# Kernel optimization log

Hardware: AMD Instinct MI355X
Metric: run time of the kernel (lower is better)

The kernel has to match this reference:

```python
import jax, jax.numpy as jnp
import numpy as np
from jax import lax

N_EXPERTS = 256
N_GROUP = 8
TOPK_GROUP = 4
TOP_K = 8
AUX_ALPHA = 0.001


def setup_inputs() -> dict:
    key = jax.random.key(0)
    k1, k2 = jax.random.split(key)
    hidden_states = jax.random.normal(k1, (16384, 2048), dtype=jnp.float32)
    weight = jax.random.normal(k2, (N_EXPERTS, 2048), dtype=jnp.float32) * 0.02
    return {"hidden_states": hidden_states, "weight": weight}


def reference(hidden_states, weight):
    n_tokens = hidden_states.shape[0]
    group_size = N_EXPERTS // N_GROUP  # 32

    # gating logits: [N, E]
    logits = jnp.einsum('nh,eh->ne', hidden_states, weight)

    # group-restricted top-k: [N, G, group_size] -> top TOPK_GROUP per group
    group_logits = logits.reshape(n_tokens, N_GROUP, group_size)
    gw, gi = lax.top_k(group_logits, TOPK_GROUP)          # [N, G, tg]
    gw = gw.reshape(n_tokens, N_GROUP * TOPK_GROUP)
    gi = gi.reshape(n_tokens, N_GROUP * TOPK_GROUP)

    # global top-k over the pooled group winners
    topk_weights, ti = lax.top_k(gw, TOP_K)               # [N, K]
    selected_group = ti // TOPK_GROUP
    expert_in_group = jnp.take_along_axis(gi, ti, axis=1)
    topk_idx = selected_group * group_size + expert_in_group  # [N, K]

    # norm_topk_prob=True
    topk_weights = topk_weights / (jnp.sum(topk_weights, axis=-1, keepdims=True) + 1e-20)

    # auxiliary load-balancing loss (training path)
    expert_mask = jax.nn.one_hot(topk_idx.reshape(-1), N_EXPERTS, dtype=jnp.float32)
    expert_counts = expert_mask.mean(axis=0)              # [E]
    expert_probs = jax.nn.softmax(logits, axis=-1).mean(axis=0)  # [E]
    aux_loss = jnp.sum(expert_counts * expert_probs) * AUX_ALPHA

    return topk_idx, topk_weights, aux_loss
```

## Files before the change

kernel.cpp:

```cpp
#include <hip/hip_runtime.h>
#include <math.h>

#define NTOK 16384
#define KD   2048
#define NE   256
#define NCHUNK 128
#define CHUNK_DW 4096
#define TM 16
#define SL 257

__global__ __launch_bounds__(256) void transform_kernel(
    const float* __restrict__ wgt, float* __restrict__ Bt)
{
    const int c    = blockIdx.x >> 2;
    const int qt   = blockIdx.x & 3;
    const int slot = qt * 256 + threadIdx.x;
    const int s    = slot >> 6;
    const int lane = slot & 63;
    const int em   = lane >> 2;
    const int l    = lane & 3;
    const int e    = (s >> 1) * 32 + (s & 1) * 16 + em;
    const float* src = wgt + (size_t)e * KD + 16 * c + l;
    float4 v = make_float4(src[0], src[4], src[8], src[12]);
    *(float4*)(Bt + (size_t)c * CHUNK_DW + slot * 4) = v;
}

typedef __attribute__((address_space(1))) const void GV;
typedef __attribute__((address_space(3))) void LV;
__device__ __forceinline__ void gld_lds16(const float* g, float* l) {
    __builtin_amdgcn_global_load_lds((GV*)g, (LV*)l, 16, 0, 0);
}

__global__ __launch_bounds__(256) void gate_kernel(
    const float* __restrict__ hid, const float* __restrict__ Bt,
    float* __restrict__ out, float* __restrict__ cnt, float* __restrict__ prb)
{
    __shared__ union { float bs[2][CHUNK_DW]; float ls[TM][SL]; } sh;
    __shared__ float As[2][TM][16];
    __shared__ float maxS[TM], sumS[TM], invS[TM];

    const int tid  = threadIdx.x;
    const int l    = tid & 3;
    const int eg   = (tid >> 2) & 31;
    const int tg   = tid >> 7;
    const int t0   = blockIdx.x * TM;
    const int lane = tid & 63;
    const int w    = tid >> 6;
    const int h    = w & 1;

    float acc[8][8];
#pragma unroll
    for (int i = 0; i < 8; ++i)
#pragma unroll
        for (int j = 0; j < 8; ++j) acc[i][j] = 0.f;

    const bool aact = (lane < 16);
    const int  at   = w * 4 + (lane >> 2);
    const int  aq   = lane & 3;
    float av[4];

    auto stageA_load = [&](int c) {
        if (aact)
            *(float4*)av = *(const float4*)(hid + (size_t)(t0 + at) * KD + 16 * c + 4 * aq);
    };
    auto stageA_write = [&](int buf) {
        if (aact) {
#pragma unroll
            for (int ll = 0; ll < 4; ++ll)
                As[buf][at][ll * 4 + aq] = av[ll];
        }
    };
    auto stageB = [&](int c, int buf) {
        const float* src = Bt + (size_t)c * CHUNK_DW + tid * 4;
        float* dst = &sh.bs[buf][tid * 4];
#pragma unroll
        for (int s = 0; s < 4; ++s)
            gld_lds16(src + s * 1024, dst + s * 1024);
    };

    stageA_load(0);
    stageB(0, 0);
    stageA_write(0);
    int cur = 0;

#pragma unroll 1
    for (int c = 0; c < NCHUNK; ++c) {
        __syncthreads();
        const int nxt = cur ^ 1;
        if (c + 1 < NCHUNK) { stageA_load(c + 1); stageB(c + 1, nxt); }

        float4 a[8];
#pragma unroll
        for (int tt = 0; tt < 8; ++tt)
            a[tt] = *(const float4*)&As[cur][tg * 8 + tt][l * 4];
#pragma unroll
        for (int j = 0; j < 8; ++j) {
            const float4 b = *(const float4*)&sh.bs[cur][((j * 2 + h) << 8) + (lane << 2)];
#pragma unroll
            for (int tt = 0; tt < 8; ++tt) {
                float s = acc[tt][j];
                s = __fadd_rn(__fmul_rn(a[tt].w, b.w), s);
                s = __fadd_rn(__fmul_rn(a[tt].z, b.z), s);
                s = __fadd_rn(__fmul_rn(a[tt].y, b.y), s);
                s = __fadd_rn(__fmul_rn(a[tt].x, b.x), s);
                acc[tt][j] = s;
            }
        }
        if (c + 1 < NCHUNK) stageA_write(nxt);
        cur = nxt;
    }

    __syncthreads();
#pragma unroll
    for (int tt = 0; tt < 8; ++tt)
#pragma unroll
        for (int j = 0; j < 8; ++j) {
            float s = acc[tt][j];
            s = __fadd_rn(s, __shfl_xor(s, 1));
            s = __fadd_rn(s, __shfl_xor(s, 2));
            if (l == 0) sh.ls[tg * 8 + tt][eg + 32 * j] = s;
        }
    if (tid < TM) sumS[tid] = 0.f;
    __syncthreads();

    if (tid < TM) {
        const float* lr = &sh.ls[tid][0];
        float tv[8]; int ti[8];
#pragma unroll
        for (int j = 0; j < 8; ++j) { tv[j] = -1e30f; ti[j] = 0; }
        float rowmax = -1e30f;

        auto ins8 = [&](float v, int idx) {
#pragma unroll
            for (int p = 0; p < 8; ++p) {
                if (v > tv[p]) {
#pragma unroll
                    for (int q = 7; q > p; --q) { tv[q] = tv[q - 1]; ti[q] = ti[q - 1]; }
                    tv[p] = v; ti[p] = idx;
                    break;
                }
            }
        };

#pragma unroll 1
        for (int g = 0; g < 8; ++g) {
            float v0 = -1e30f, v1 = -1e30f, v2 = -1e30f, v3 = -1e30f;
            int   i0 = 0, i1 = 0, i2 = 0, i3 = 0;
            for (int j = 0; j < 32; ++j) {
                const float v = lr[g * 32 + j];
                if (v > v0)      { v3=v2;i3=i2; v2=v1;i2=i1; v1=v0;i1=i0; v0=v;i0=j; }
                else if (v > v1) { v3=v2;i3=i2; v2=v1;i2=i1; v1=v;i1=j; }
                else if (v > v2) { v3=v2;i3=i2; v2=v;i2=j; }
                else if (v > v3) { v3=v;i3=j; }
            }
            rowmax = fmaxf(rowmax, v0);
            ins8(v0, g * 32 + i0);
            ins8(v1, g * 32 + i1);
            ins8(v2, g * 32 + i2);
            ins8(v3, g * 32 + i3);
        }

        const float s01 = __fadd_rn(tv[0], tv[1]);
        const float s23 = __fadd_rn(tv[2], tv[3]);
        const float s45 = __fadd_rn(tv[4], tv[5]);
        const float s67 = __fadd_rn(tv[6], tv[7]);
        float s = __fadd_rn(__fadd_rn(s01, s23), __fadd_rn(s45, s67));
        s = __fadd_rn(s, 1e-20f);

        const size_t tg2 = (size_t)(t0 + tid);
#pragma unroll
        for (int j = 0; j < 8; ++j) {
            out[tg2 * 8 + j]                    = (float)ti[j];
            out[(size_t)NTOK * 8 + tg2 * 8 + j] = __fdiv_rn(tv[j], s);
            atomicAdd(&cnt[ti[j]], 1.0f);
        }
        maxS[tid] = rowmax;
    }
    __syncthreads();

    {
        const int t  = tid >> 4;
        const int c0 = (tid & 15) * 16;
        const float m = maxS[t];
        float part = 0.f;
#pragma unroll
        for (int j = 0; j < 16; ++j) part += __expf(sh.ls[t][c0 + j] - m);
        atomicAdd(&sumS[t], part);
    }
    __syncthreads();
    if (tid < TM) invS[tid] = 1.0f / sumS[tid];
    __syncthreads();

    {
        float p = 0.f;
#pragma unroll
        for (int n = 0; n < TM; ++n) p += __expf(sh.ls[n][tid] - maxS[n]) * invS[n];
        atomicAdd(&prb[tid], p);
    }
}

__global__ void aux_kernel(const float* __restrict__ cnt,
                           const float* __restrict__ prb,
                           float* __restrict__ out)
{
    const int tid = threadIdx.x;
    float v = cnt[tid] * prb[tid];
#pragma unroll
    for (int off = 32; off; off >>= 1) v += __shfl_down(v, off, 64);
    __shared__ float ps[4];
    if ((tid & 63) == 0) ps[tid >> 6] = v;
    __syncthreads();
    if (tid == 0) {
        const float tot = ps[0] + ps[1] + ps[2] + ps[3];
        out[(size_t)NTOK * 8 * 2] = tot * (0.001f / (131072.0f * 16384.0f));
    }
}

extern "C" void kernel_launch(void* const* d_in, const int* in_sizes, int n_in,
                              void* d_out, int out_size, void* d_ws, size_t ws_size,
                              hipStream_t stream)
{
    (void)in_sizes; (void)n_in; (void)out_size; (void)ws_size;
    const float* hid = (const float*)d_in[0];
    const float* wgt = (const float*)d_in[1];
    float* out = (float*)d_out;
    float* cnt = (float*)d_ws;
    float* prb = cnt + NE;
    float* Bt  = prb + NE;

    hipMemsetAsync(d_ws, 0, 2 * NE * sizeof(float), stream);
    transform_kernel<<<512, 256, 0, stream>>>(wgt, Bt);
    gate_kernel<<<NTOK / TM, 256, 0, stream>>>(hid, Bt, out, cnt, prb);
    aux_kernel<<<1, 256, 0, stream>>>(cnt, prb, out);
}
```

Before: 552.3 us.

## Use packed FP32 mul/add with 32-token tiles and 512-thread blocks

Replaces the scalar mul-then-add inner loop with v_pk_mul_f32/v_pk_add_f32 inline asm. Each packed op now processes two tokens at once against a broadcast weight element, with separate mul and add kept so rounding is unchanged. The A tile in shared memory is re-laid out so adjacent token pairs are interleaved, which makes the packed operands load directly. Block size doubles to 512 threads with 32 tokens per block, and the B-stage copy uses two loads per thread instead of four. The aim is to halve VALU instruction count for the GEMV-like gating matmul, at the cost of register pressure from the occupancy hint and a longer serial top-k epilogue per block.

After: 534.7 us. 3.2% less time.

```diff
diff --git a/kernel.cpp b/kernel.cpp
--- a/kernel.cpp
+++ b/kernel.cpp
@@ -6,8 +6,28 @@
 #define NE   256
 #define NCHUNK 128
 #define CHUNK_DW 4096
-#define TM 16
+#define TM 32
 #define SL 257
+
+typedef float f32x2 __attribute__((ext_vector_type(2)));
+
+__device__ __forceinline__ f32x2 pk_mul_lo(f32x2 a, f32x2 b) {
+    f32x2 d;
+    asm("v_pk_mul_f32 %0, %1, %2 op_sel:[0,0] op_sel_hi:[1,0]"
+        : "=v"(d) : "v"(a), "v"(b));
+    return d;
+}
+__device__ __forceinline__ f32x2 pk_mul_hi(f32x2 a, f32x2 b) {
+    f32x2 d;
+    asm("v_pk_mul_f32 %0, %1, %2 op_sel:[0,1] op_sel_hi:[1,1]"
+        : "=v"(d) : "v"(a), "v"(b));
+    return d;
+}
+__device__ __forceinline__ f32x2 pk_add(f32x2 a, f32x2 b) {
+    f32x2 d;
+    asm("v_pk_add_f32 %0, %1, %2" : "=v"(d) : "v"(a), "v"(b));
+    return d;
+}
 
 __global__ __launch_bounds__(256) void transform_kernel(
     const float* __restrict__ wgt, float* __restrict__ Bt)
@@ -31,12 +51,12 @@
     __builtin_amdgcn_global_load_lds((GV*)g, (LV*)l, 16, 0, 0);
 }
 
-__global__ __launch_bounds__(256) void gate_kernel(
+__global__ __launch_bounds__(512, 4) void gate_kernel(
     const float* __restrict__ hid, const float* __restrict__ Bt,
     float* __restrict__ out, float* __restrict__ cnt, float* __restrict__ prb)
 {
     __shared__ union { float bs[2][CHUNK_DW]; float ls[TM][SL]; } sh;
-    __shared__ float As[2][TM][16];
+    __shared__ float As2[2][4][132];
     __shared__ float maxS[TM], sumS[TM], invS[TM];
 
     const int tid  = threadIdx.x;
@@ -48,11 +68,11 @@
     const int w    = tid >> 6;
     const int h    = w & 1;
 
-    float acc[8][8];
-#pragma unroll
-    for (int i = 0; i < 8; ++i)
-#pragma unroll
-        for (int j = 0; j < 8; ++j) acc[i][j] = 0.f;
+    f32x2 acc2[4][8];
+#pragma unroll
+    for (int i = 0; i < 4; ++i)
+#pragma unroll
+        for (int j = 0; j < 8; ++j) acc2[i][j] = (f32x2){0.f, 0.f};
 
     const bool aact = (lane < 16);
     const int  at   = w * 4 + (lane >> 2);
@@ -65,17 +85,17 @@
     };
     auto stageA_write = [&](int buf) {
         if (aact) {
+            const int base = (at >> 1) * 8 + aq * 2 + (at & 1);
 #pragma unroll
             for (int ll = 0; ll < 4; ++ll)
-                As[buf][at][ll * 4 + aq] = av[ll];
+                As2[buf][ll][base] = av[ll];
         }
     };
     auto stageB = [&](int c, int buf) {
         const float* src = Bt + (size_t)c * CHUNK_DW + tid * 4;
         float* dst = &sh.bs[buf][tid * 4];
-#pragma unroll
-        for (int s = 0; s < 4; ++s)
-            gld_lds16(src + s * 1024, dst + s * 1024);
+        gld_lds16(src, dst);
+        gld_lds16(src + 2048, dst + 2048);
     };
 
     stageA_load(0);
@@ -89,21 +109,30 @@
         const int nxt = cur ^ 1;
         if (c + 1 < NCHUNK) { stageA_load(c + 1); stageB(c + 1, nxt); }
 
-        float4 a[8];
-#pragma unroll
-        for (int tt = 0; tt < 8; ++tt)
-            a[tt] = *(const float4*)&As[cur][tg * 8 + tt][l * 4];
+        float4 ar0[4], ar1[4];
+#pragma unroll
+        for (int tp = 0; tp < 4; ++tp) {
+            const float* ap = &As2[cur][l][(tg * 4 + tp) * 8];
+            ar0[tp] = *(const float4*)(ap);
+            ar1[tp] = *(const float4*)(ap + 4);
+        }
 #pragma unroll
         for (int j = 0; j < 8; ++j) {
             const float4 b = *(const float4*)&sh.bs[cur][((j * 2 + h) << 8) + (lane << 2)];
-#pragma unroll
-            for (int tt = 0; tt < 8; ++tt) {
-                float s = acc[tt][j];
-                s = __fadd_rn(__fmul_rn(a[tt].w, b.w), s);
-                s = __fadd_rn(__fmul_rn(a[tt].z, b.z), s);
-                s = __fadd_rn(__fmul_rn(a[tt].y, b.y), s);
-                s = __fadd_rn(__fmul_rn(a[tt].x, b.x), s);
-                acc[tt][j] = s;
+            const f32x2 b01 = (f32x2){b.x, b.y};
+            const f32x2 b23 = (f32x2){b.z, b.w};
+#pragma unroll
+            for (int tp = 0; tp < 4; ++tp) {
+                const f32x2 aQ0 = (f32x2){ar0[tp].x, ar0[tp].y};
+                const f32x2 aQ1 = (f32x2){ar0[tp].z, ar0[tp].w};
+                const f32x2 aQ2 = (f32x2){ar1[tp].x, ar1[tp].y};
+                const f32x2 aQ3 = (f32x2){ar1[tp].z, ar1[tp].w};
+                f32x2 s = acc2[tp][j];
+                s = pk_add(pk_mul_hi(aQ3, b23), s);
+                s = pk_add(pk_mul_lo(aQ2, b23), s);
+                s = pk_add(pk_mul_hi(aQ1, b01), s);
+                s = pk_add(pk_mul_lo(aQ0, b01), s);
+                acc2[tp][j] = s;
             }
         }
         if (c + 1 < NCHUNK) stageA_write(nxt);
@@ -112,13 +141,18 @@
 
     __syncthreads();
 #pragma unroll
-    for (int tt = 0; tt < 8; ++tt)
+    for (int tp = 0; tp < 4; ++tp)
 #pragma unroll
         for (int j = 0; j < 8; ++j) {
-            float s = acc[tt][j];
-            s = __fadd_rn(s, __shfl_xor(s, 1));
-            s = __fadd_rn(s, __shfl_xor(s, 2));
-            if (l == 0) sh.ls[tg * 8 + tt][eg + 32 * j] = s;
+            float sx = acc2[tp][j].x, sy = acc2[tp][j].y;
+            sx = __fadd_rn(sx, __shfl_xor(sx, 1));
+            sx = __fadd_rn(sx, __shfl_xor(sx, 2));
+            sy = __fadd_rn(sy, __shfl_xor(sy, 1));
+            sy = __fadd_rn(sy, __shfl_xor(sy, 2));
+            if (l == 0) {
+                sh.ls[tg * 8 + 2 * tp][eg + 32 * j]     = sx;
+                sh.ls[tg * 8 + 2 * tp + 1][eg + 32 * j] = sy;
+            }
         }
     if (tid < TM) sumS[tid] = 0.f;
     __syncthreads();
@@ -191,7 +225,7 @@
     if (tid < TM) invS[tid] = 1.0f / sumS[tid];
     __syncthreads();
 
-    {
+    if (tid < NE) {
         float p = 0.f;
 #pragma unroll
         for (int n = 0; n < TM; ++n) p += __expf(sh.ls[n][tid] - maxS[n]) * invS[n];
@@ -230,6 +264,6 @@
 
     hipMemsetAsync(d_ws, 0, 2 * NE * sizeof(float), stream);
     transform_kernel<<<512, 256, 0, stream>>>(wgt, Bt);
-    gate_kernel<<<NTOK / TM, 256, 0, stream>>>(hid, Bt, out, cnt, prb);
+    gate_kernel<<<NTOK / TM, 512, 0, stream>>>(hid, Bt, out, cnt, prb);
     aux_kernel<<<1, 256, 0, stream>>>(cnt, prb, out);
 }
```
